# Kernel optimization log

Measured on AMD Instinct MI355X. Metric: run time of the kernel, lower is better.

## Reference

```python
import jax, jax.numpy as jnp
import numpy as np

ALPHA = 0.2  # LeakyReLU negative slope

def setup_inputs() -> dict:
    key = jax.random.key(0)
    k1, k2, k3 = jax.random.split(key, 3)
    B, N, D_in, D_out = 4, 512, 512, 256
    H = jax.random.normal(k1, (B, N, D_in), dtype=jnp.float32)
    # xavier-style scaled params
    W = jax.random.normal(k2, (D_out, D_in), dtype=jnp.float32) * (2.0 / (D_in + D_out)) ** 0.5
    a = jax.random.normal(k3, (D_out, 1), dtype=jnp.float32) * (2.0 / (D_out + 1)) ** 0.5
    return {"H": H, "W": W, "a": a}

def reference(H, W, a):
    # Wh: [B, N, D_out]
    Wh = jnp.einsum('bnd,od->bno', H, W)
    # additive pairwise scores: e[b,i,j] = leakyrelu(Wh[b,i]+Wh[b,j]) . a
    e = jnp.einsum('bijo,o->bij',
                   jax.nn.leaky_relu(Wh[:, :, None, :] + Wh[:, None, :, :], ALPHA),
                   a[:, 0])
    attention = jax.nn.softmax(e, axis=-1)          # [B, N, N]
    H_att = jnp.einsum('bij,bjo->bio', attention, Wh)  # [B, N, D_out]
    return H_att
```

## Files before the change

### kernel.cpp

```cpp
#include <hip/hip_runtime.h>

constexpr int Bq   = 4;
constexpr int Nq   = 512;
constexpr int DIN  = 512;
constexpr int DOUT = 256;

typedef _Float16 h2  __attribute__((ext_vector_type(2)));
typedef _Float16 h8  __attribute__((ext_vector_type(8)));
typedef float    f4v __attribute__((ext_vector_type(4)));
typedef float    v2f __attribute__((ext_vector_type(2)));

#if defined(__has_builtin) && __has_builtin(__builtin_amdgcn_fdot2)
__device__ __forceinline__ float fdot2f(h2 a, h2 b, float c) {
    return __builtin_amdgcn_fdot2(a, b, c, false);
}
#else
__device__ __forceinline__ float fdot2f(h2 a, h2 b, float c) {
    return (float)a.x * (float)b.x + (float)a.y * (float)b.y + c;
}
#endif

__device__ __forceinline__ h8 cvt8(float4 lo, float4 hi) {
    h8 r;
    r[0] = (_Float16)lo.x; r[1] = (_Float16)lo.y;
    r[2] = (_Float16)lo.z; r[3] = (_Float16)lo.w;
    r[4] = (_Float16)hi.x; r[5] = (_Float16)hi.y;
    r[6] = (_Float16)hi.z; r[7] = (_Float16)hi.w;
    return r;
}

__global__ __launch_bounds__(256) void k1_wh(const float* __restrict__ H,
                                             const float* __restrict__ W,
                                             const float* __restrict__ a,
                                             float* __restrict__ Wh,
                                             h2* __restrict__ Wh16,
                                             h2* __restrict__ WhT16p,
                                             h2* __restrict__ a16) {
    const int bid = blockIdx.x;
    const int t   = threadIdx.x;

    if (bid == 512) {
        if (t < 64) {
            const int idx = 2 * t;
            const float4 v = *(const float4*)&a[2 * idx];
            h2 h0; h0.x = (_Float16)v.x; h0.y = (_Float16)v.y;
            h2 h1; h1.x = (_Float16)v.z; h1.y = (_Float16)v.w;
            a16[idx] = h0; a16[idx + 1] = h1;
        }
        return;
    }

    const int w    = t >> 6;
    const int lane = t & 63;
    const int mt   = bid >> 2;
    const int b    = mt & 3;
    const int n0   = (mt >> 2) << 4;
    const int o0   = ((bid & 3) << 6) + (w << 4);
    const int quad = lane >> 4;
    const int col  = lane & 15;

    const float4* __restrict__ aP =
        (const float4*)(H + (size_t)(b * Nq + n0 + col) * DIN) + quad * 2;
    const float4* __restrict__ bP =
        (const float4*)(W + (size_t)(o0 + col) * DIN) + quad * 2;

    f4v acc = {0.f, 0.f, 0.f, 0.f};
    float4 fa0 = aP[0], fa1 = aP[1];
    float4 fb0 = bP[0], fb1 = bP[1];

#pragma unroll
    for (int kb = 0; kb < 16; ++kb) {
        float4 na0 = fa0, na1 = fa1, nb0 = fb0, nb1 = fb1;
        if (kb < 15) {
            na0 = aP[(kb + 1) * 8];
            na1 = aP[(kb + 1) * 8 + 1];
            nb0 = bP[(kb + 1) * 8];
            nb1 = bP[(kb + 1) * 8 + 1];
        }
        const h8 af = cvt8(fa0, fa1);
        const h8 bf = cvt8(fb0, fb1);
        acc = __builtin_amdgcn_mfma_f32_16x16x32_f16(af, bf, acc, 0, 0, 0);
        fa0 = na0; fa1 = na1; fb0 = nb0; fb1 = nb1;
    }

    const int rowb = b * Nq + n0 + quad * 4;
#pragma unroll
    for (int reg = 0; reg < 4; ++reg) {
        const float v = acc[reg];
        Wh[(size_t)(rowb + reg) * DOUT + o0 + col] = v;
        const float vp = __shfl_xor(v, 1);
        if ((col & 1) == 0) {
            h2 hv; hv.x = (_Float16)v; hv.y = (_Float16)vp;
            const int o2 = (o0 + col) >> 1;
            Wh16[(size_t)(rowb + reg) * 128 + o2] = hv;
            WhT16p[(size_t)b * 65536 + (size_t)o2 * 512 + (n0 + quad * 4 + reg)] = hv;
        }
    }
}

__global__ __launch_bounds__(1024, 8) void k23(const float* __restrict__ Wh,
                                               const h2* __restrict__ Wh16,
                                               const h2* __restrict__ WhT16p,
                                               const h2* __restrict__ a16,
                                               float* __restrict__ out) {
    const int t   = threadIdx.x;
    const int blk = blockIdx.x;
    const int b   = blk & 3;
    const int i0  = (blk >> 2) << 2;

    __shared__ float smem[8192];
    __shared__ float sP[4 * 512];
    __shared__ float wred[2][4][8];

    {
        const int h  = __builtin_amdgcn_readfirstlane(t >> 9);
        const int j  = t & 511;
        const int ob = h * 64;

        const h2* __restrict__ wjp = WhT16p + (size_t)b * 65536 + (size_t)ob * 512 + j;
        const h2* __restrict__ wip = Wh16 + (size_t)(b * Nq + i0) * 128;

        float ab[4] = {0.f, 0.f, 0.f, 0.f};
        float rja = 0.f;
        h2 cA[8], cB[8];

#define K2_L8(buf, kb)                                                      \
    _Pragma("unroll") for (int s = 0; s < 8; ++s)                           \
        buf[s] = wjp[((kb) + s) * 512];

#define K2_C8(buf, kb)                                                      \
    _Pragma("unroll") for (int s = 0; s < 8; ++s) {                         \
        const int o2 = ob + (kb) + s;                                       \
        const h2 a2 = a16[o2];                                  \
        rja = fdot2f(a2, buf[s], rja);                                      \
        _Pragma("unroll") for (int rr = 0; rr < 4; ++rr) {                  \
            const h2 wi = wip[rr * 128 + o2];                   \
            h2 w  = buf[s] + wi;                                \
            h2 aw = __builtin_elementwise_max(w, -w);           \
            ab[rr] = fdot2f(a2, aw, ab[rr]);                    \
        }                                                                   \
    }

        K2_L8(cA, 0)  K2_L8(cB, 8)
        K2_C8(cA, 0)  K2_L8(cA, 16)
        K2_C8(cB, 8)  K2_L8(cB, 24)
        K2_C8(cA, 16) K2_L8(cA, 32)
        K2_C8(cB, 24) K2_L8(cB, 40)
        K2_C8(cA, 32) K2_L8(cA, 48)
        K2_C8(cB, 40) K2_L8(cB, 56)
        K2_C8(cA, 48)
        K2_C8(cB, 56)
#undef K2_L8
#undef K2_C8

        float* sAb = smem;
        float* sRh = smem + 2048;
        float* sRf = smem + 2560;
        if (h == 1) {
#pragma unroll
            for (int rr = 0; rr < 4; ++rr) sAb[rr * 512 + j] = ab[rr];
            sRh[j] = rja;
        }
        __syncthreads();

        float rj = 0.f;
        if (h == 0) {
#pragma unroll
            for (int rr = 0; rr < 4; ++rr) ab[rr] += sAb[rr * 512 + j];
            rj = rja + sRh[j];
            sRf[j] = rj;
        }
        __syncthreads();

        float e[4], pv[4];
        const int lane = t & 63;
        const int w    = t >> 6;

        if (h == 0) {
#pragma unroll
            for (int rr = 0; rr < 4; ++rr)
                e[rr] = 0.6f * (sRf[i0 + rr] + rj) + 0.4f * ab[rr];
#pragma unroll
            for (int rr = 0; rr < 4; ++rr) {
                float v = e[rr];
#pragma unroll
                for (int off = 32; off > 0; off >>= 1) v = fmaxf(v, __shfl_xor(v, off));
                if (lane == 0) wred[0][rr][w] = v;
            }
        }
        __syncthreads();
        if (h == 0) {
#pragma unroll
            for (int rr = 0; rr < 4; ++rr) {
                const float4 q0 = *(const float4*)&wred[0][rr][0];
                const float4 q1 = *(const float4*)&wred[0][rr][4];
                const float m = fmaxf(fmaxf(fmaxf(q0.x, q0.y), fmaxf(q0.z, q0.w)),
                                      fmaxf(fmaxf(q1.x, q1.y), fmaxf(q1.z, q1.w)));
                pv[rr] = __expf(e[rr] - m);
            }
#pragma unroll
            for (int rr = 0; rr < 4; ++rr) {
                float v = pv[rr];
#pragma unroll
                for (int off = 32; off > 0; off >>= 1) v += __shfl_xor(v, off);
                if (lane == 0) wred[1][rr][w] = v;
            }
        }
        __syncthreads();
        if (h == 0) {
#pragma unroll
            for (int rr = 0; rr < 4; ++rr) {
                const float4 q0 = *(const float4*)&wred[1][rr][0];
                const float4 q1 = *(const float4*)&wred[1][rr][4];
                const float s = (q0.x + q0.y + q0.z + q0.w) + (q1.x + q1.y + q1.z + q1.w);
                sP[rr * 512 + j] = pv[rr] * (1.0f / s);
            }
        }
        __syncthreads();
    }

    {
        const int w16 = __builtin_amdgcn_readfirstlane(t >> 6);
        const int oq  = t & 63;
        const int jb  = w16 * 32;

        const float4* __restrict__ wh4 = (const float4*)(Wh + (size_t)b * Nq * DOUT) + oq;

        f4v acc[4];
#pragma unroll
        for (int rr = 0; rr < 4; ++rr) acc[rr] = (f4v)0.f;

#pragma unroll 2
        for (int s = 0; s < 8; ++s) {
            const int j = jb + s * 4;
            const float4 w0 = wh4[(j + 0) * 64];
            const float4 w1 = wh4[(j + 1) * 64];
            const float4 w2 = wh4[(j + 2) * 64];
            const float4 w3 = wh4[(j + 3) * 64];
            const f4v v0 = {w0.x, w0.y, w0.z, w0.w};
            const f4v v1 = {w1.x, w1.y, w1.z, w1.w};
            const f4v v2 = {w2.x, w2.y, w2.z, w2.w};
            const f4v v3 = {w3.x, w3.y, w3.z, w3.w};
#pragma unroll
            for (int rr = 0; rr < 4; ++rr) {
                const float4 p4 = *(const float4*)&sP[rr * 512 + j];
                acc[rr] = __builtin_elementwise_fma((f4v)p4.x, v0, acc[rr]);
                acc[rr] = __builtin_elementwise_fma((f4v)p4.y, v1, acc[rr]);
                acc[rr] = __builtin_elementwise_fma((f4v)p4.z, v2, acc[rr]);
                acc[rr] = __builtin_elementwise_fma((f4v)p4.w, v3, acc[rr]);
            }
        }

        float4* sPart = (float4*)smem;
        if (w16 >= 8) {
#pragma unroll
            for (int rr = 0; rr < 4; ++rr) {
                float4 f;
                f.x = acc[rr][0]; f.y = acc[rr][1]; f.z = acc[rr][2]; f.w = acc[rr][3];
                sPart[((w16 - 8) * 4 + rr) * 64 + oq] = f;
            }
        }
        __syncthreads();
        if (w16 < 8) {
#pragma unroll
            for (int rr = 0; rr < 4; ++rr) {
                const int idx = (w16 * 4 + rr) * 64 + oq;
                const float4 v = sPart[idx];
                float4 f;
                f.x = acc[rr][0] + v.x; f.y = acc[rr][1] + v.y;
                f.z = acc[rr][2] + v.z; f.w = acc[rr][3] + v.w;
                sPart[idx] = f;
            }
        }
        __syncthreads();

        if (t < 256) {
            const int row = t >> 6, oqq = t & 63;
            f4v fin = (f4v)0.f;
#pragma unroll
            for (int k = 0; k < 8; ++k) {
                const float4 v = sPart[(k * 4 + row) * 64 + oqq];
                fin[0] += v.x; fin[1] += v.y; fin[2] += v.z; fin[3] += v.w;
            }
            float4 f;
            f.x = fin[0]; f.y = fin[1]; f.z = fin[2]; f.w = fin[3];
            ((float4*)(out + ((size_t)(b * Nq) + i0 + row) * DOUT))[oqq] = f;
        }
    }
}

extern "C" void kernel_launch(void* const* d_in, const int* in_sizes, int n_in,
                              void* d_out, int out_size, void* d_ws, size_t ws_size,
                              hipStream_t stream) {
    const float* H = (const float*)d_in[0];
    const float* W = (const float*)d_in[1];
    const float* a = (const float*)d_in[2];
    float* out = (float*)d_out;

    float* Wh  = (float*)d_ws;
    h2* Wh16   = (h2*)(Wh + 524288);
    h2* WhT16p = Wh16 + 262144;
    h2* a16    = WhT16p + 262144;

    hipLaunchKernelGGL(k1_wh, dim3(513), dim3(256),  0, stream, H, W, a, Wh, Wh16, WhT16p, a16);
    hipLaunchKernelGGL(k23,   dim3(512), dim3(1024), 0, stream, Wh, Wh16, WhT16p, a16, out);
}
```

Before: 101.9 us.

## Use MFMA for attention-weighted sum, 8 rows per block, split-K projection

The final P·Wh product now runs on fp16 MFMA instead of fp32 FMAs, reading a new transposed fp16 copy of Wh and fp16 probabilities stored in LDS. Each k23 block handles 8 query rows instead of 4, halving the grid and reusing each j-column load across more rows. The projection kernel splits K across wave pairs and reduces through LDS to double its block count. The fp32 Wh buffer is dropped. Fp16 probabilities reduce accuracy, and half of each MFMA tile's rows are wasted because only 8 rows are valid.

Measured after the change: 107.5 us. +5.4%, slower.

```diff
diff --git a/kernel.cpp b/kernel.cpp
--- a/kernel.cpp
+++ b/kernel.cpp
@@ -6,9 +6,9 @@
 constexpr int DOUT = 256;
 
 typedef _Float16 h2  __attribute__((ext_vector_type(2)));
+typedef _Float16 h4  __attribute__((ext_vector_type(4)));
 typedef _Float16 h8  __attribute__((ext_vector_type(8)));
 typedef float    f4v __attribute__((ext_vector_type(4)));
-typedef float    v2f __attribute__((ext_vector_type(2)));
 
 #if defined(__has_builtin) && __has_builtin(__builtin_amdgcn_fdot2)
 __device__ __forceinline__ float fdot2f(h2 a, h2 b, float c) {
@@ -32,14 +32,14 @@
 __global__ __launch_bounds__(256) void k1_wh(const float* __restrict__ H,
                                              const float* __restrict__ W,
                                              const float* __restrict__ a,
-                                             float* __restrict__ Wh,
                                              h2* __restrict__ Wh16,
                                              h2* __restrict__ WhT16p,
+                                             h2* __restrict__ WhT16n,
                                              h2* __restrict__ a16) {
     const int bid = blockIdx.x;
     const int t   = threadIdx.x;
 
-    if (bid == 512) {
+    if (bid == 1024) {
         if (t < 64) {
             const int idx = 2 * t;
             const float4 v = *(const float4*)&a[2 * idx];
@@ -52,26 +52,28 @@
 
     const int w    = t >> 6;
     const int lane = t & 63;
-    const int mt   = bid >> 2;
+    const int T    = (bid << 1) | (w & 1);
+    const int kh   = w >> 1;
+    const int mt   = T >> 4;
     const int b    = mt & 3;
-    const int n0   = (mt >> 2) << 4;
-    const int o0   = ((bid & 3) << 6) + (w << 4);
+    const int n0   = (T >> 6) << 4;
+    const int o0   = (T & 15) << 4;
     const int quad = lane >> 4;
     const int col  = lane & 15;
 
     const float4* __restrict__ aP =
-        (const float4*)(H + (size_t)(b * Nq + n0 + col) * DIN) + quad * 2;
+        (const float4*)(H + (size_t)(b * Nq + n0 + col) * DIN) + kh * 64 + quad * 2;
     const float4* __restrict__ bP =
-        (const float4*)(W + (size_t)(o0 + col) * DIN) + quad * 2;
+        (const float4*)(W + (size_t)(o0 + col) * DIN) + kh * 64 + quad * 2;
 
     f4v acc = {0.f, 0.f, 0.f, 0.f};
     float4 fa0 = aP[0], fa1 = aP[1];
     float4 fb0 = bP[0], fb1 = bP[1];
 
 #pragma unroll
-    for (int kb = 0; kb < 16; ++kb) {
+    for (int kb = 0; kb < 8; ++kb) {
         float4 na0 = fa0, na1 = fa1, nb0 = fb0, nb1 = fb1;
-        if (kb < 15) {
+        if (kb < 7) {
             na0 = aP[(kb + 1) * 8];
             na1 = aP[(kb + 1) * 8 + 1];
             nb0 = bP[(kb + 1) * 8];
@@ -83,34 +85,48 @@
         fa0 = na0; fa1 = na1; fb0 = nb0; fb1 = nb1;
     }
 
-    const int rowb = b * Nq + n0 + quad * 4;
-#pragma unroll
-    for (int reg = 0; reg < 4; ++reg) {
-        const float v = acc[reg];
-        Wh[(size_t)(rowb + reg) * DOUT + o0 + col] = v;
-        const float vp = __shfl_xor(v, 1);
-        if ((col & 1) == 0) {
-            h2 hv; hv.x = (_Float16)v; hv.y = (_Float16)vp;
-            const int o2 = (o0 + col) >> 1;
-            Wh16[(size_t)(rowb + reg) * 128 + o2] = hv;
-            WhT16p[(size_t)b * 65536 + (size_t)o2 * 512 + (n0 + quad * 4 + reg)] = hv;
-        }
-    }
-}
-
-__global__ __launch_bounds__(1024, 8) void k23(const float* __restrict__ Wh,
-                                               const h2* __restrict__ Wh16,
+    __shared__ f4v sPart[2][64];
+    if (kh) sPart[w & 1][lane] = acc;
+    __syncthreads();
+    if (!kh) {
+        const f4v p = sPart[w & 1][lane];
+#pragma unroll
+        for (int r = 0; r < 4; ++r) acc[r] += p[r];
+
+        const int rloc = n0 + quad * 4;
+
+        h4 hj;
+        hj[0] = (_Float16)acc[0]; hj[1] = (_Float16)acc[1];
+        hj[2] = (_Float16)acc[2]; hj[3] = (_Float16)acc[3];
+        *(h4*)(WhT16n + ((size_t)(b * 256 + o0 + col)) * 256 + (rloc >> 1)) = hj;
+
+#pragma unroll
+        for (int reg = 0; reg < 4; ++reg) {
+            const float v  = acc[reg];
+            const float vp = __shfl_xor(v, 1);
+            if ((col & 1) == 0) {
+                h2 hv; hv.x = (_Float16)v; hv.y = (_Float16)vp;
+                const int o2 = (o0 + col) >> 1;
+                Wh16[(size_t)(b * Nq + rloc + reg) * 128 + o2] = hv;
+                WhT16p[(size_t)b * 65536 + (size_t)o2 * 512 + (rloc + reg)] = hv;
+            }
+        }
+    }
+}
+
+__global__ __launch_bounds__(1024, 8) void k23(const h2* __restrict__ Wh16,
                                                const h2* __restrict__ WhT16p,
+                                               const h2* __restrict__ WhT16n,
                                                const h2* __restrict__ a16,
                                                float* __restrict__ out) {
     const int t   = threadIdx.x;
     const int blk = blockIdx.x;
     const int b   = blk & 3;
-    const int i0  = (blk >> 2) << 2;
-
-    __shared__ float smem[8192];
-    __shared__ float sP[4 * 512];
-    __shared__ float wred[2][4][8];
+    const int i0  = (blk >> 2) << 3;
+
+    __shared__ float smem[5120];
+    __shared__ h2    sPh[8 * 260];
+    __shared__ float wred[2][8][8];
 
     {
         const int h  = __builtin_amdgcn_readfirstlane(t >> 9);
@@ -120,7 +136,9 @@
         const h2* __restrict__ wjp = WhT16p + (size_t)b * 65536 + (size_t)ob * 512 + j;
         const h2* __restrict__ wip = Wh16 + (size_t)(b * Nq + i0) * 128;
 
-        float ab[4] = {0.f, 0.f, 0.f, 0.f};
+        float ab[8];
+#pragma unroll
+        for (int rr = 0; rr < 8; ++rr) ab[rr] = 0.f;
         float rja = 0.f;
         h2 cA[8], cB[8];
 
@@ -133,7 +151,7 @@
         const int o2 = ob + (kb) + s;                                       \
         const h2 a2 = a16[o2];                                  \
         rja = fdot2f(a2, buf[s], rja);                                      \
-        _Pragma("unroll") for (int rr = 0; rr < 4; ++rr) {                  \
+        _Pragma("unroll") for (int rr = 0; rr < 8; ++rr) {                  \
             const h2 wi = wip[rr * 128 + o2];                   \
             h2 w  = buf[s] + wi;                                \
             h2 aw = __builtin_elementwise_max(w, -w);           \
@@ -154,11 +172,11 @@
 #undef K2_C8
 
         float* sAb = smem;
-        float* sRh = smem + 2048;
-        float* sRf = smem + 2560;
+        float* sRh = smem + 4096;
+        float* sRf = smem + 4608;
         if (h == 1) {
 #pragma unroll
-            for (int rr = 0; rr < 4; ++rr) sAb[rr * 512 + j] = ab[rr];
+            for (int rr = 0; rr < 8; ++rr) sAb[rr * 512 + j] = ab[rr];
             sRh[j] = rja;
         }
         __syncthreads();
@@ -166,22 +184,22 @@
         float rj = 0.f;
         if (h == 0) {
 #pragma unroll
-            for (int rr = 0; rr < 4; ++rr) ab[rr] += sAb[rr * 512 + j];
+            for (int rr = 0; rr < 8; ++rr) ab[rr] += sAb[rr * 512 + j];
             rj = rja + sRh[j];
             sRf[j] = rj;
         }
         __syncthreads();
 
-        float e[4], pv[4];
+        float e[8], pv[8];
         const int lane = t & 63;
         const int w    = t >> 6;
 
         if (h == 0) {
 #pragma unroll
-            for (int rr = 0; rr < 4; ++rr)
+            for (int rr = 0; rr < 8; ++rr)
                 e[rr] = 0.6f * (sRf[i0 + rr] + rj) + 0.4f * ab[rr];
 #pragma unroll
-            for (int rr = 0; rr < 4; ++rr) {
+            for (int rr = 0; rr < 8; ++rr) {
                 float v = e[rr];
 #pragma unroll
                 for (int off = 32; off > 0; off >>= 1) v = fmaxf(v, __shfl_xor(v, off));
@@ -191,7 +209,7 @@
         __syncthreads();
         if (h == 0) {
 #pragma unroll
-            for (int rr = 0; rr < 4; ++rr) {
+            for (int rr = 0; rr < 8; ++rr) {
                 const float4 q0 = *(const float4*)&wred[0][rr][0];
                 const float4 q1 = *(const float4*)&wred[0][rr][4];
                 const float m = fmaxf(fmaxf(fmaxf(q0.x, q0.y), fmaxf(q0.z, q0.w)),
@@ -199,7 +217,7 @@
                 pv[rr] = __expf(e[rr] - m);
             }
 #pragma unroll
-            for (int rr = 0; rr < 4; ++rr) {
+            for (int rr = 0; rr < 8; ++rr) {
                 float v = pv[rr];
 #pragma unroll
                 for (int off = 32; off > 0; off >>= 1) v += __shfl_xor(v, off);
@@ -209,82 +227,49 @@
         __syncthreads();
         if (h == 0) {
 #pragma unroll
-            for (int rr = 0; rr < 4; ++rr) {
+            for (int rr = 0; rr < 8; ++rr) {
                 const float4 q0 = *(const float4*)&wred[1][rr][0];
                 const float4 q1 = *(const float4*)&wred[1][rr][4];
                 const float s = (q0.x + q0.y + q0.z + q0.w) + (q1.x + q1.y + q1.z + q1.w);
-                sP[rr * 512 + j] = pv[rr] * (1.0f / s);
+                const float pn = pv[rr] * (1.0f / s);
+                const float pp = __shfl_xor(pn, 1);
+                if ((j & 1) == 0) {
+                    h2 hv; hv.x = (_Float16)pn; hv.y = (_Float16)pp;
+                    sPh[rr * 260 + (j >> 1)] = hv;
+                }
             }
         }
         __syncthreads();
     }
 
     {
-        const int w16 = __builtin_amdgcn_readfirstlane(t >> 6);
-        const int oq  = t & 63;
-        const int jb  = w16 * 32;
-
-        const float4* __restrict__ wh4 = (const float4*)(Wh + (size_t)b * Nq * DOUT) + oq;
-
-        f4v acc[4];
-#pragma unroll
-        for (int rr = 0; rr < 4; ++rr) acc[rr] = (f4v)0.f;
-
-#pragma unroll 2
-        for (int s = 0; s < 8; ++s) {
-            const int j = jb + s * 4;
-            const float4 w0 = wh4[(j + 0) * 64];
-            const float4 w1 = wh4[(j + 1) * 64];
-            const float4 w2 = wh4[(j + 2) * 64];
-            const float4 w3 = wh4[(j + 3) * 64];
-            const f4v v0 = {w0.x, w0.y, w0.z, w0.w};
-            const f4v v1 = {w1.x, w1.y, w1.z, w1.w};
-            const f4v v2 = {w2.x, w2.y, w2.z, w2.w};
-            const f4v v3 = {w3.x, w3.y, w3.z, w3.w};
-#pragma unroll
-            for (int rr = 0; rr < 4; ++rr) {
-                const float4 p4 = *(const float4*)&sP[rr * 512 + j];
-                acc[rr] = __builtin_elementwise_fma((f4v)p4.x, v0, acc[rr]);
-                acc[rr] = __builtin_elementwise_fma((f4v)p4.y, v1, acc[rr]);
-                acc[rr] = __builtin_elementwise_fma((f4v)p4.z, v2, acc[rr]);
-                acc[rr] = __builtin_elementwise_fma((f4v)p4.w, v3, acc[rr]);
-            }
-        }
-
-        float4* sPart = (float4*)smem;
-        if (w16 >= 8) {
-#pragma unroll
-            for (int rr = 0; rr < 4; ++rr) {
-                float4 f;
-                f.x = acc[rr][0]; f.y = acc[rr][1]; f.z = acc[rr][2]; f.w = acc[rr][3];
-                sPart[((w16 - 8) * 4 + rr) * 64 + oq] = f;
-            }
-        }
-        __syncthreads();
-        if (w16 < 8) {
-#pragma unroll
-            for (int rr = 0; rr < 4; ++rr) {
-                const int idx = (w16 * 4 + rr) * 64 + oq;
-                const float4 v = sPart[idx];
-                float4 f;
-                f.x = acc[rr][0] + v.x; f.y = acc[rr][1] + v.y;
-                f.z = acc[rr][2] + v.z; f.w = acc[rr][3] + v.w;
-                sPart[idx] = f;
-            }
-        }
-        __syncthreads();
-
-        if (t < 256) {
-            const int row = t >> 6, oqq = t & 63;
-            f4v fin = (f4v)0.f;
-#pragma unroll
-            for (int k = 0; k < 8; ++k) {
-                const float4 v = sPart[(k * 4 + row) * 64 + oqq];
-                fin[0] += v.x; fin[1] += v.y; fin[2] += v.z; fin[3] += v.w;
-            }
-            float4 f;
-            f.x = fin[0]; f.y = fin[1]; f.z = fin[2]; f.w = fin[3];
-            ((float4*)(out + ((size_t)(b * Nq) + i0 + row) * DOUT))[oqq] = f;
+        const int w16  = __builtin_amdgcn_readfirstlane(t >> 6);
+        const int lane = t & 63;
+        const int quad = lane >> 4;
+        const int col  = lane & 15;
+        const int o0   = w16 << 4;
+
+        const h2* __restrict__ wt =
+            WhT16n + (size_t)b * 65536 + (size_t)(o0 + col) * 256 + quad * 4;
+        const h2* __restrict__ ap = sPh + (col & 7) * 260 + quad * 4;
+
+        f4v acc = {0.f, 0.f, 0.f, 0.f};
+        h8 b0 = *(const h8*)wt;
+#pragma unroll
+        for (int kb = 0; kb < 16; ++kb) {
+            h8 b1 = b0;
+            if (kb < 15) b1 = *(const h8*)(wt + (kb + 1) * 16);
+            const h8 af = *(const h8*)(ap + kb * 16);
+            acc = __builtin_amdgcn_mfma_f32_16x16x32_f16(af, b0, acc, 0, 0, 0);
+            b0 = b1;
+        }
+
+        if (quad < 2) {
+#pragma unroll
+            for (int reg = 0; reg < 4; ++reg) {
+                const int row = quad * 4 + reg;
+                out[((size_t)(b * Nq) + i0 + row) * DOUT + o0 + col] = acc[reg];
+            }
         }
     }
 }
@@ -297,11 +282,11 @@
     const float* a = (const float*)d_in[2];
     float* out = (float*)d_out;
 
-    float* Wh  = (float*)d_ws;
-    h2* Wh16   = (h2*)(Wh + 524288);
+    h2* Wh16   = (h2*)d_ws;
     h2* WhT16p = Wh16 + 262144;
-    h2* a16    = WhT16p + 262144;
-
-    hipLaunchKernelGGL(k1_wh, dim3(513), dim3(256),  0, stream, H, W, a, Wh, Wh16, WhT16p, a16);
-    hipLaunchKernelGGL(k23,   dim3(512), dim3(1024), 0, stream, Wh, Wh16, WhT16p, a16, out);
-}
+    h2* WhT16n = WhT16p + 262144;
+    h2* a16    = WhT16n + 262144;
+
+    hipLaunchKernelGGL(k1_wh, dim3(1025), dim3(256),  0, stream, H, W, a, Wh16, WhT16p, WhT16n, a16);
+    hipLaunchKernelGGL(k23,   dim3(256),  dim3(1024), 0, stream, Wh16, WhT16p, WhT16n, a16, out);
+}
```
